# Kernel tuning notes

Measured on AMD Instinct MI355X. Metric: run time of the kernel, lower is better.

## Reference

```python
import jax, jax.numpy as jnp
import numpy as np

INPUT_DIM = 1024
EMBED_DIM = 1024
NUM_HEADS = 16
HEAD_DIM = EMBED_DIM // NUM_HEADS


def _xavier_uniform(key, shape):
    fan_in, fan_out = shape[1], shape[0]
    limit = float(np.sqrt(6.0 / (fan_in + fan_out)))
    return jax.random.uniform(key, shape, jnp.float32, -limit, limit)


def setup_inputs() -> dict:
    key = jax.random.key(0)
    kx, kqkv, ko = jax.random.split(key, 3)
    return {
        "x": jax.random.normal(kx, (2, 2048, INPUT_DIM), jnp.float32),
        "qkv_w": _xavier_uniform(kqkv, (3 * EMBED_DIM, INPUT_DIM)),
        "qkv_b": jnp.zeros((3 * EMBED_DIM,), jnp.float32),
        "o_w": _xavier_uniform(ko, (EMBED_DIM, INPUT_DIM)),
        "o_b": jnp.zeros((EMBED_DIM,), jnp.float32),
    }


def reference(x, qkv_w, qkv_b, o_w, o_b):
    B, S, _ = x.shape
    scale = HEAD_DIM ** -0.5
    # fused QKV projection: [B,S,3E]
    qkv = jnp.einsum('bsd,ed->bse', x, qkv_w) + qkv_b
    # [B,S,H,3Dh] -> [B,H,S,3Dh], then split into q,k,v
    qkv = qkv.reshape(B, S, NUM_HEADS, 3 * HEAD_DIM).transpose(0, 2, 1, 3)
    q, k, v = jnp.split(qkv, 3, axis=-1)
    # scaled dot-product attention
    scores = jnp.einsum('bhqd,bhkd->bhqk', q, k) * scale
    attn = jax.nn.softmax(scores, axis=-1)
    values = jnp.einsum('bhqk,bhkd->bhqd', attn, v)
    # [B,H,S,Dh] -> [B,S,E]
    values = values.transpose(0, 2, 1, 3).reshape(B, S, EMBED_DIM)
    return jnp.einsum('bse,oe->bso', values, o_w) + o_b
```

## Files before the change

kernel.cpp:

```cpp
#include <hip/hip_runtime.h>
#include <hip/hip_bf16.h>

typedef __bf16  bf16x8 __attribute__((ext_vector_type(8)));
typedef __bf16  bf16x2 __attribute__((ext_vector_type(2)));
typedef float   f32x4  __attribute__((ext_vector_type(4)));

#define LOG2E 1.44269504088896340736f

__device__ __forceinline__ void async_copy16(const void* g, void* l) {
  __builtin_amdgcn_global_load_lds(
      (const __attribute__((address_space(1))) unsigned int*)g,
      (__attribute__((address_space(3))) unsigned int*)l, 16, 0, 0);
}

__global__ void detect_dtype(const unsigned int* __restrict__ w, int* __restrict__ flag) {
  __shared__ int cnt;
  if (threadIdx.x == 0) cnt = 0;
  __syncthreads();
  unsigned int v = w[threadIdx.x];
  if (v & 0x4000u) atomicAdd(&cnt, 1);
  __syncthreads();
  if (threadIdx.x == 0) *flag = (cnt > 16) ? 1 : 0;
}

#define C0 524288
#define C1 393216
#define C2 384
#define C3 131072
#define C4 128
#define CTOT (C0 + C1 + C2 + C3 + C4)
__global__ void convert_all(const void* __restrict__ x,  const void* __restrict__ qw,
                            const void* __restrict__ qb, const void* __restrict__ ow,
                            const void* __restrict__ ob,
                            __bf16* __restrict__ cx,  __bf16* __restrict__ cqw,
                            __bf16* __restrict__ cqb, __bf16* __restrict__ cow,
                            __bf16* __restrict__ cob, const int* __restrict__ flag) {
  const int f = *flag;
  int i = blockIdx.x * blockDim.x + threadIdx.x;
  const int stride = gridDim.x * blockDim.x;
  for (; i < CTOT; i += stride) {
    const void* s; __bf16* d; int off;
    if      (i < C0)                { s = x;  d = cx;  off = i; }
    else if (i < C0 + C1)           { s = qw; d = cqw; off = i - C0; }
    else if (i < C0 + C1 + C2)      { s = qb; d = cqb; off = i - C0 - C1; }
    else if (i < C0 + C1 + C2 + C3) { s = ow; d = cow; off = i - C0 - C1 - C2; }
    else                            { s = ob; d = cob; off = i - C0 - C1 - C2 - C3; }
    if (f) {
      const f32x4* sp = (const f32x4*)s;
      f32x4 a = sp[2 * off], b = sp[2 * off + 1];
      bf16x8 o;
      o[0] = (__bf16)a[0]; o[1] = (__bf16)a[1]; o[2] = (__bf16)a[2]; o[3] = (__bf16)a[3];
      o[4] = (__bf16)b[0]; o[5] = (__bf16)b[1]; o[6] = (__bf16)b[2]; o[7] = (__bf16)b[3];
      *(bf16x8*)&d[8 * off] = o;
    } else {
      *(bf16x8*)&d[8 * off] = ((const bf16x8*)s)[off];
    }
  }
}

template<int BN>
__global__ __launch_bounds__(256) void gemm_nt_bias(
    const __bf16* __restrict__ A,
    const __bf16* __restrict__ Bt,
    const __bf16* __restrict__ bias,
    __bf16* __restrict__ Cb,
    float* __restrict__ Cf,
    const int* __restrict__ flag,
    int M, int N, int K)
{
  constexpr int NI    = BN / 32;
  constexpr int BITER = (BN * 4) / 256;
  __shared__ __align__(16) __bf16 As[128 * 32];
  __shared__ __align__(16) __bf16 Bs[BN * 32];

  const int tid  = threadIdx.x;
  const int lane = tid & 63;
  const int wave = tid >> 6;
  const int qd   = lane >> 4;
  const int ln   = lane & 15;
  const int m0 = blockIdx.y * 128;
  const int n0 = blockIdx.x * BN;
  const int wm = (wave >> 1) * 64;
  const int wn = (wave & 1) * (16 * NI);

  f32x4 acc[4][NI] = {};

  for (int kt = 0; kt < K; kt += 32) {
#pragma unroll
    for (int i = 0; i < 2; ++i) {
      int s  = wave * 128 + i * 64 + lane;
      int r  = s >> 2;
      int cb = s & 3;
      async_copy16(A + (size_t)(m0 + r) * K + kt + cb * 8, &As[(wave * 128 + i * 64) * 8]);
    }
#pragma unroll
    for (int i = 0; i < BITER; ++i) {
      int s  = wave * (64 * BITER) + i * 64 + lane;
      int r  = s >> 2;
      int cb = s & 3;
      async_copy16(Bt + (size_t)(n0 + r) * K + kt + cb * 8,
                   &Bs[(wave * (64 * BITER) + i * 64) * 8]);
    }
    __syncthreads();

    bf16x8 af[4], bfr[NI];
#pragma unroll
    for (int t = 0; t < 4; ++t)
      af[t] = *(const bf16x8*)&As[(wm + t * 16 + ln) * 32 + qd * 8];
#pragma unroll
    for (int t = 0; t < NI; ++t)
      bfr[t] = *(const bf16x8*)&Bs[(wn + t * 16 + ln) * 32 + qd * 8];
#pragma unroll
    for (int mi = 0; mi < 4; ++mi)
#pragma unroll
      for (int ni = 0; ni < NI; ++ni)
        acc[mi][ni] = __builtin_amdgcn_mfma_f32_16x16x32_bf16(af[mi], bfr[ni], acc[mi][ni], 0, 0, 0);
    __syncthreads();
  }

  const bool f32out = (Cf != nullptr) && (*flag != 0);
#pragma unroll
  for (int ni = 0; ni < NI; ++ni) {
    int col = n0 + wn + ni * 16 + ln;
    float bv = (float)bias[col];
#pragma unroll
    for (int mi = 0; mi < 4; ++mi) {
#pragma unroll
      for (int r = 0; r < 4; ++r) {
        int row = m0 + wm + mi * 16 + qd * 4 + r;
        float v = acc[mi][ni][r] + bv;
        if (f32out) Cf[(size_t)row * N + col] = v;
        else        Cb[(size_t)row * N + col] = (__bf16)v;
      }
    }
  }
}

#define AST 76
#define PST 72
__global__ __launch_bounds__(256) void attn_flash(
    const __bf16* __restrict__ qkv,
    __bf16* __restrict__ vals)
{
  __shared__ __align__(16) __bf16 Qs[128 * AST];
  __shared__ __align__(16) __bf16 Ks[64 * AST];
  __shared__ __align__(16) __bf16 Vt[64 * AST];
  __shared__ __align__(16) __bf16 Ps[4][32 * PST];

  const int tid  = threadIdx.x;
  const int lane = tid & 63;
  const int wave = tid >> 6;
  const int qd   = lane >> 4;
  const int ln   = lane & 15;
  const int b  = blockIdx.y >> 4;
  const int h  = blockIdx.y & 15;
  const int q0 = blockIdx.x * 128;
  const __bf16* base = qkv + (size_t)b * 2048 * 3072 + h * 192;

#pragma unroll
  for (int i = 0; i < 4; ++i) {
    int s  = tid + i * 256;
    int r  = s >> 3;
    int cb = s & 7;
    bf16x8 v = *(const bf16x8*)&base[(size_t)(q0 + r) * 3072 + cb * 8];
    *(bf16x8*)&Qs[r * AST + cb * 8] = v;
  }

  const float kScale = 0.125f * LOG2E;

  f32x4 oaccT[2][4] = {};
  float lpart[2] = {0.f, 0.f};

  for (int kt = 0; kt < 2048; kt += 64) {
    bf16x8 kv[2];
#pragma unroll
    for (int i = 0; i < 2; ++i) {
      int s = tid + i * 256;
      int r = s >> 3, cb = s & 7;
      kv[i] = *(const bf16x8*)&base[(size_t)(kt + r) * 3072 + 64 + cb * 8];
    }
    const int p  = tid & 31;
    const int db = (tid >> 5) * 8;
    const __bf16* g0 = base + (size_t)(kt + 2 * p) * 3072 + 128 + db;
    bf16x8 v0 = *(const bf16x8*)g0;
    bf16x8 v1 = *(const bf16x8*)(g0 + 3072);

    __syncthreads();
#pragma unroll
    for (int i = 0; i < 2; ++i) {
      int s = tid + i * 256;
      int r = s >> 3, cb = s & 7;
      *(bf16x8*)&Ks[r * AST + cb * 8] = kv[i];
    }
#pragma unroll
    for (int i = 0; i < 8; ++i) {
      bf16x2 w; w[0] = v0[i]; w[1] = v1[i];
      *(bf16x2*)&Vt[(db + i) * AST + 2 * p] = w;
    }
    __syncthreads();

    f32x4 sacc[2][4] = {};
#pragma unroll
    for (int ks = 0; ks < 2; ++ks) {
      bf16x8 kfr[4], qfr[2];
#pragma unroll
      for (int mi = 0; mi < 4; ++mi)
        kfr[mi] = *(const bf16x8*)&Ks[(mi * 16 + ln) * AST + ks * 32 + qd * 8];
#pragma unroll
      for (int nt = 0; nt < 2; ++nt)
        qfr[nt] = *(const bf16x8*)&Qs[(wave * 32 + nt * 16 + ln) * AST + ks * 32 + qd * 8];
#pragma unroll
      for (int nt = 0; nt < 2; ++nt)
#pragma unroll
        for (int mi = 0; mi < 4; ++mi)
          sacc[nt][mi] = __builtin_amdgcn_mfma_f32_16x16x32_bf16(kfr[mi], qfr[nt], sacc[nt][mi], 0, 0, 0);
    }

    __bf16* P = Ps[wave];
#pragma unroll
    for (int nt = 0; nt < 2; ++nt) {
      float rs = 0.f;
#pragma unroll
      for (int mi = 0; mi < 4; ++mi) {
        float pv[4];
#pragma unroll
        for (int r = 0; r < 4; ++r) {
          pv[r] = __builtin_exp2f(sacc[nt][mi][r] * kScale);
          rs += pv[r];
        }
#pragma unroll
        for (int t = 0; t < 2; ++t) {
          bf16x2 w; w[0] = (__bf16)pv[2 * t]; w[1] = (__bf16)pv[2 * t + 1];
          *(bf16x2*)&P[(nt * 16 + ln) * PST + mi * 16 + qd * 4 + 2 * t] = w;
        }
      }
      lpart[nt] += rs;
    }

    asm volatile("s_waitcnt lgkmcnt(0)" ::: "memory");

#pragma unroll
    for (int ks = 0; ks < 2; ++ks) {
      bf16x8 vfr[4], pfr[2];
#pragma unroll
      for (int md = 0; md < 4; ++md)
        vfr[md] = *(const bf16x8*)&Vt[(md * 16 + ln) * AST + ks * 32 + qd * 8];
#pragma unroll
      for (int nt = 0; nt < 2; ++nt)
        pfr[nt] = *(const bf16x8*)&P[(nt * 16 + ln) * PST + ks * 32 + qd * 8];
#pragma unroll
      for (int nt = 0; nt < 2; ++nt)
#pragma unroll
        for (int md = 0; md < 4; ++md)
          oaccT[nt][md] = __builtin_amdgcn_mfma_f32_16x16x32_bf16(vfr[md], pfr[nt], oaccT[nt][md], 0, 0, 0);
    }
  }

#pragma unroll
  for (int nt = 0; nt < 2; ++nt) {
    float l = lpart[nt];
    l += __shfl_xor(l, 16);
    l += __shfl_xor(l, 32);
    float il = 1.0f / l;
    int row = q0 + wave * 32 + nt * 16 + ln;
    __bf16* o = vals + ((size_t)b * 2048 + row) * 1024 + h * 64;
#pragma unroll
    for (int md = 0; md < 4; ++md)
#pragma unroll
      for (int r = 0; r < 4; ++r)
        o[md * 16 + qd * 4 + r] = (__bf16)(oaccT[nt][md][r] * il);
  }
}

extern "C" void kernel_launch(void* const* d_in, const int* in_sizes, int n_in,
                              void* d_out, int out_size, void* d_ws, size_t ws_size,
                              hipStream_t stream) {
  __bf16* ws    = (__bf16*)d_ws;
  __bf16* qkv   = ws;
  __bf16* vals  = qkv   + (size_t)4096 * 3072;
  __bf16* cx    = vals  + (size_t)4096 * 1024;
  __bf16* cqkvw = cx    + (size_t)4096 * 1024;
  __bf16* cow   = cqkvw + (size_t)3072 * 1024;
  __bf16* cqkvb = cow   + (size_t)1024 * 1024;
  __bf16* cob   = cqkvb + 4096;
  int*    flag  = (int*)(cob + 4096);

  dim3 blk(256);

  detect_dtype<<<1, 256, 0, stream>>>((const unsigned int*)d_in[1], flag);

  convert_all<<<1024, 256, 0, stream>>>(d_in[0], d_in[1], d_in[2], d_in[3], d_in[4],
                                        cx, cqkvw, cqkvb, cow, cob, flag);

  gemm_nt_bias<128><<<dim3(3072 / 128, 4096 / 128), blk, 0, stream>>>(
      cx, cqkvw, cqkvb, qkv, nullptr, flag, 4096, 3072, 1024);

  attn_flash<<<dim3(2048 / 128, 32), blk, 0, stream>>>(qkv, vals);

  gemm_nt_bias<64><<<dim3(1024 / 64, 4096 / 128), blk, 0, stream>>>(
      vals, cow, cob, (__bf16*)d_out, (float*)d_out, flag, 4096, 1024, 1024);
}
```

Measured before the change: 228.1 us.

## Keep Q in registers, async-copy swizzled K to LDS, fold dtype detection

The attention kernel now loads its Q fragments straight into registers instead of staging them in LDS. K tiles are copied with global_load_lds into an XOR-swizzled unpadded layout rather than passing through registers, and V/P use a narrower padded stride with 4-wide P stores. The separate dtype-detection kernel is merged into the conversion kernel, which removes one launch. The aim is less LDS traffic and fewer launches and register round-trips, at the cost of a higher register count and reliance on the async copy being complete when the existing barrier is reached.

```diff
diff --git a/kernel.cpp b/kernel.cpp
--- a/kernel.cpp
+++ b/kernel.cpp
@@ -2,6 +2,7 @@
 #include <hip/hip_bf16.h>
 
 typedef __bf16  bf16x8 __attribute__((ext_vector_type(8)));
+typedef __bf16  bf16x4 __attribute__((ext_vector_type(4)));
 typedef __bf16  bf16x2 __attribute__((ext_vector_type(2)));
 typedef float   f32x4  __attribute__((ext_vector_type(4)));
 
@@ -11,16 +12,6 @@
   __builtin_amdgcn_global_load_lds(
       (const __attribute__((address_space(1))) unsigned int*)g,
       (__attribute__((address_space(3))) unsigned int*)l, 16, 0, 0);
-}
-
-__global__ void detect_dtype(const unsigned int* __restrict__ w, int* __restrict__ flag) {
-  __shared__ int cnt;
-  if (threadIdx.x == 0) cnt = 0;
-  __syncthreads();
-  unsigned int v = w[threadIdx.x];
-  if (v & 0x4000u) atomicAdd(&cnt, 1);
-  __syncthreads();
-  if (threadIdx.x == 0) *flag = (cnt > 16) ? 1 : 0;
 }
 
 #define C0 524288
@@ -34,8 +25,16 @@
                             const void* __restrict__ ob,
                             __bf16* __restrict__ cx,  __bf16* __restrict__ cqw,
                             __bf16* __restrict__ cqb, __bf16* __restrict__ cow,
-                            __bf16* __restrict__ cob, const int* __restrict__ flag) {
-  const int f = *flag;
+                            __bf16* __restrict__ cob, int* __restrict__ flag) {
+  __shared__ int cnt;
+  if (threadIdx.x == 0) cnt = 0;
+  __syncthreads();
+  unsigned int w = ((const unsigned int*)qw)[threadIdx.x];
+  if (w & 0x4000u) atomicAdd(&cnt, 1);
+  __syncthreads();
+  const int f = (cnt > 16) ? 1 : 0;
+  if (threadIdx.x == 0) *flag = f;
+
   int i = blockIdx.x * blockDim.x + threadIdx.x;
   const int stride = gridDim.x * blockDim.x;
   for (; i < CTOT; i += stride) {
@@ -136,15 +135,13 @@
   }
 }
 
-#define AST 76
 #define PST 72
 __global__ __launch_bounds__(256) void attn_flash(
     const __bf16* __restrict__ qkv,
     __bf16* __restrict__ vals)
 {
-  __shared__ __align__(16) __bf16 Qs[128 * AST];
-  __shared__ __align__(16) __bf16 Ks[64 * AST];
-  __shared__ __align__(16) __bf16 Vt[64 * AST];
+  __shared__ __align__(16) __bf16 Ks[64 * 64];
+  __shared__ __align__(16) __bf16 Vt[64 * PST];
   __shared__ __align__(16) __bf16 Ps[4][32 * PST];
 
   const int tid  = threadIdx.x;
@@ -157,14 +154,13 @@
   const int q0 = blockIdx.x * 128;
   const __bf16* base = qkv + (size_t)b * 2048 * 3072 + h * 192;
 
-#pragma unroll
-  for (int i = 0; i < 4; ++i) {
-    int s  = tid + i * 256;
-    int r  = s >> 3;
-    int cb = s & 7;
-    bf16x8 v = *(const bf16x8*)&base[(size_t)(q0 + r) * 3072 + cb * 8];
-    *(bf16x8*)&Qs[r * AST + cb * 8] = v;
-  }
+  bf16x8 qfr[2][2];
+#pragma unroll
+  for (int nt = 0; nt < 2; ++nt)
+#pragma unroll
+    for (int ks = 0; ks < 2; ++ks)
+      qfr[nt][ks] = *(const bf16x8*)&base[(size_t)(q0 + wave * 32 + nt * 16 + ln) * 3072
+                                          + ks * 32 + qd * 8];
 
   const float kScale = 0.125f * LOG2E;
 
@@ -172,13 +168,6 @@
   float lpart[2] = {0.f, 0.f};
 
   for (int kt = 0; kt < 2048; kt += 64) {
-    bf16x8 kv[2];
-#pragma unroll
-    for (int i = 0; i < 2; ++i) {
-      int s = tid + i * 256;
-      int r = s >> 3, cb = s & 7;
-      kv[i] = *(const bf16x8*)&base[(size_t)(kt + r) * 3072 + 64 + cb * 8];
-    }
     const int p  = tid & 31;
     const int db = (tid >> 5) * 8;
     const __bf16* g0 = base + (size_t)(kt + 2 * p) * 3072 + 128 + db;
@@ -186,34 +175,36 @@
     bf16x8 v1 = *(const bf16x8*)(g0 + 3072);
 
     __syncthreads();
+
 #pragma unroll
     for (int i = 0; i < 2; ++i) {
-      int s = tid + i * 256;
-      int r = s >> 3, cb = s & 7;
-      *(bf16x8*)&Ks[r * AST + cb * 8] = kv[i];
+      int s   = wave * 64 + i * 256 + lane;
+      int r   = s >> 3;
+      int xcb = (s & 7) ^ (r & 7);
+      async_copy16(base + (size_t)(kt + r) * 3072 + 64 + xcb * 8,
+                   &Ks[(wave * 64 + i * 256) * 8]);
     }
 #pragma unroll
     for (int i = 0; i < 8; ++i) {
       bf16x2 w; w[0] = v0[i]; w[1] = v1[i];
-      *(bf16x2*)&Vt[(db + i) * AST + 2 * p] = w;
+      *(bf16x2*)&Vt[(db + i) * PST + 2 * p] = w;
     }
     __syncthreads();
 
     f32x4 sacc[2][4] = {};
 #pragma unroll
     for (int ks = 0; ks < 2; ++ks) {
-      bf16x8 kfr[4], qfr[2];
-#pragma unroll
-      for (int mi = 0; mi < 4; ++mi)
-        kfr[mi] = *(const bf16x8*)&Ks[(mi * 16 + ln) * AST + ks * 32 + qd * 8];
+      bf16x8 kfr[4];
+#pragma unroll
+      for (int mi = 0; mi < 4; ++mi) {
+        int row = mi * 16 + ln;
+        kfr[mi] = *(const bf16x8*)&Ks[row * 64 + (((ks * 4 + qd) ^ (row & 7)) * 8)];
+      }
 #pragma unroll
       for (int nt = 0; nt < 2; ++nt)
-        qfr[nt] = *(const bf16x8*)&Qs[(wave * 32 + nt * 16 + ln) * AST + ks * 32 + qd * 8];
-#pragma unroll
-      for (int nt = 0; nt < 2; ++nt)
 #pragma unroll
         for (int mi = 0; mi < 4; ++mi)
-          sacc[nt][mi] = __builtin_amdgcn_mfma_f32_16x16x32_bf16(kfr[mi], qfr[nt], sacc[nt][mi], 0, 0, 0);
+          sacc[nt][mi] = __builtin_amdgcn_mfma_f32_16x16x32_bf16(kfr[mi], qfr[nt][ks], sacc[nt][mi], 0, 0, 0);
     }
 
     __bf16* P = Ps[wave];
@@ -228,11 +219,10 @@
           pv[r] = __builtin_exp2f(sacc[nt][mi][r] * kScale);
           rs += pv[r];
         }
-#pragma unroll
-        for (int t = 0; t < 2; ++t) {
-          bf16x2 w; w[0] = (__bf16)pv[2 * t]; w[1] = (__bf16)pv[2 * t + 1];
-          *(bf16x2*)&P[(nt * 16 + ln) * PST + mi * 16 + qd * 4 + 2 * t] = w;
-        }
+        bf16x4 w;
+        w[0] = (__bf16)pv[0]; w[1] = (__bf16)pv[1];
+        w[2] = (__bf16)pv[2]; w[3] = (__bf16)pv[3];
+        *(bf16x4*)&P[(nt * 16 + ln) * PST + mi * 16 + qd * 4] = w;
       }
       lpart[nt] += rs;
     }
@@ -244,7 +234,7 @@
       bf16x8 vfr[4], pfr[2];
 #pragma unroll
       for (int md = 0; md < 4; ++md)
-        vfr[md] = *(const bf16x8*)&Vt[(md * 16 + ln) * AST + ks * 32 + qd * 8];
+        vfr[md] = *(const bf16x8*)&Vt[(md * 16 + ln) * PST + ks * 32 + qd * 8];
 #pragma unroll
       for (int nt = 0; nt < 2; ++nt)
         pfr[nt] = *(const bf16x8*)&P[(nt * 16 + ln) * PST + ks * 32 + qd * 8];
@@ -287,8 +277,6 @@
 
   dim3 blk(256);
 
-  detect_dtype<<<1, 256, 0, stream>>>((const unsigned int*)d_in[1], flag);
-
   convert_all<<<1024, 256, 0, stream>>>(d_in[0], d_in[1], d_in[2], d_in[3], d_in[4],
                                         cx, cqkvw, cqkvb, cow, cob, flag);
 
```

Result: faster. 216.5 us (-5.1%).
